# Kernel optimization log

Hardware: AMD Instinct MI355X
Metric: run time of the kernel (lower is better)

The kernel has to match this reference:

```python
import jax, jax.numpy as jnp
import numpy as np

N_NODES = 100000


def _gcn_conv(x, edge_index, W, b, n_nodes):
    # PyG GCNConv with add_self_loops=True, default gcn_norm:
    #   out = D^{-1/2} (A + I) D^{-1/2} (x @ W) + b
    xw = x @ W  # [N, out_dim]
    src = jnp.concatenate([edge_index[0], jnp.arange(n_nodes)])
    dst = jnp.concatenate([edge_index[1], jnp.arange(n_nodes)])
    ones = jnp.ones(src.shape[0], dtype=x.dtype)
    deg = jax.ops.segment_sum(ones, dst, num_segments=n_nodes)  # includes self loops
    dinv = jnp.where(deg > 0, jax.lax.rsqrt(deg), 0.0)
    norm = dinv[src] * dinv[dst]  # [E + N]
    msgs = xw[src] * norm[:, None]  # gather + scale per edge
    out = jax.ops.segment_sum(msgs, dst, num_segments=n_nodes)
    return out + b


def setup_inputs() -> dict:
    key = jax.random.key(0)
    k1, k2, k3, k4 = jax.random.split(key, 4)
    N, E = N_NODES, 1600000
    in_dim, hid_dim, out_dim = 128, 128, 64
    x = jax.random.normal(k1, (N, in_dim), dtype=jnp.float32)
    edge_index = jax.random.randint(k2, (2, E), 0, N, dtype=jnp.int64)
    W1 = jax.random.normal(k3, (in_dim, hid_dim), dtype=jnp.float32) * (1.0 / np.sqrt(in_dim))
    b1 = jnp.zeros((hid_dim,), dtype=jnp.float32)
    W2 = jax.random.normal(k4, (hid_dim, out_dim), dtype=jnp.float32) * (1.0 / np.sqrt(hid_dim))
    b2 = jnp.zeros((out_dim,), dtype=jnp.float32)
    return {"x": x, "edge_index": edge_index, "W1": W1, "b1": b1, "W2": W2, "b2": b2}


def reference(x, edge_index, W1, b1, W2, b2):
    h = _gcn_conv(x, edge_index, W1, b1, N_NODES)
    out = _gcn_conv(h, edge_index, W2, b2, N_NODES)
    return out
```

## Files before the change

### kernel.cpp

```cpp
#include <hip/hip_runtime.h>

#define NNODES 100000
#define NBUCK ((NNODES + 127) >> 7)
#define CAPB 3072
#define QCAP 1024
#define BINCAP 16
#define GFILL 256

typedef __attribute__((ext_vector_type(8))) short short8;
typedef __attribute__((ext_vector_type(4))) float f32x4;

__device__ __forceinline__ float bf2f(unsigned short u) {
    unsigned int v = ((unsigned int)u) << 16;
    return __builtin_bit_cast(float, v);
}
__device__ __forceinline__ unsigned short f2bf(float f) {
    unsigned int u = __builtin_bit_cast(unsigned int, f);
    u += 0x7FFF + ((u >> 16) & 1);
    return (unsigned short)(u >> 16);
}


__global__ __launch_bounds__(512) void fill_wc(const int* __restrict__ ei, int E,
                                               int* __restrict__ gcur,
                                               int* __restrict__ seg,
                                               int* __restrict__ deg) {
    __shared__ int lcnt[NBUCK];
    __shared__ int lbin[NBUCK * BINCAP];

    const int t = threadIdx.x;
    for (int i = t; i < NBUCK; i += 512) lcnt[i] = 0;
    __syncthreads();

    const int per = (E + GFILL - 1) / GFILL;
    const int e0 = blockIdx.x * per;
    const int e1 = min(e0 + per, E);

    for (int base = e0; base < e1; base += 512) {
        int e = base + t;
        if (e < e1) {
            int src = ei[e];
            int d = ei[E + e];
            atomicAdd(&deg[d], 1);
            int b = (unsigned)d >> 7;
            int p = (src << 7) | (d & 127);
            int pos = atomicAdd(&lcnt[b], 1);
            if (pos < BINCAP) {
                lbin[b * BINCAP + pos] = p;
            } else {
                int gp = atomicAdd(&gcur[b << 4], 1);
                if (gp < CAPB) seg[b * CAPB + gp] = p;
            }
        }
        __syncthreads();
        for (int bb = t; bb < NBUCK; bb += 512) {
            if (lcnt[bb] >= BINCAP) {
                int gp = atomicAdd(&gcur[bb << 4], BINCAP);
                if (gp + BINCAP <= CAPB) {
                    int* dp = seg + bb * CAPB + gp;
                    const int* sp = lbin + bb * BINCAP;
#pragma unroll
                    for (int j = 0; j < BINCAP; ++j) dp[j] = sp[j];
                }
                lcnt[bb] = 0;
            }
        }
        __syncthreads();
    }
    for (int bb = t; bb < NBUCK; bb += 512) {
        int c = min(lcnt[bb], BINCAP);
        if (c > 0) {
            int gp = atomicAdd(&gcur[bb << 4], c);
            int* dp = seg + bb * CAPB;
            const int* sp = lbin + bb * BINCAP;
            for (int j = 0; j < c && gp + j < CAPB; ++j) dp[gp + j] = sp[j];
        }
    }
}


__global__ __launch_bounds__(256) void w12_kernel(const float* __restrict__ W1,
                                                  const float* __restrict__ b1,
                                                  const float* __restrict__ W2,
                                                  float* __restrict__ W12,
                                                  float* __restrict__ bW2,
                                                  unsigned short* __restrict__ whi,
                                                  unsigned short* __restrict__ wlo) {
    int j = threadIdx.x % 64;
    int r = threadIdx.x / 64;
    if (blockIdx.x < 32) {
        int i = blockIdx.x * 4 + r;
        float acc = 0.f;
        for (int k = 0; k < 128; ++k) acc += W1[i * 128 + k] * W2[k * 64 + j];
        W12[i * 64 + j] = acc;
        int kc = i >> 5;
        int ik = i & 31;
        int lane = ((ik >> 3) << 4) | (j & 15);
        int jj = ik & 7;
        int nt = j >> 4;
        size_t idx = (size_t)(((nt << 2) | kc) * 64 + lane) * 8 + jj;
        unsigned short h = f2bf(acc);
        whi[idx] = h;
        wlo[idx] = f2bf(acc - bf2f(h));
    } else if (r == 0) {
        float acc = 0.f;
        for (int k = 0; k < 128; ++k) acc += b1[k] * W2[k * 64 + j];
        bW2[j] = acc;
    }
}


__global__ __launch_bounds__(256) void gemm_mfma(const float* __restrict__ X,
                                                 const unsigned short* __restrict__ whi,
                                                 const unsigned short* __restrict__ wlo,
                                                 const int* __restrict__ deg,
                                                 unsigned short* __restrict__ Ybf, int N) {
    const int tid = threadIdx.x;
    const int wv = tid >> 6;
    const int l = tid & 63;
    const int lm = l & 15;
    const int lk = l >> 4;
    const int rowbase = blockIdx.x * 64 + wv * 16;
    const int arow = min(rowbase + lm, N - 1);

    const float* xp = X + (size_t)arow * 128 + lk * 8;

    f32x4 acc[4];
#pragma unroll
    for (int nt = 0; nt < 4; ++nt) acc[nt] = (f32x4){0.f, 0.f, 0.f, 0.f};

#pragma unroll
    for (int kc = 0; kc < 4; ++kc) {
        float4 xa = *(const float4*)(xp + kc * 32);
        float4 xb = *(const float4*)(xp + kc * 32 + 4);
        float xs[8] = {xa.x, xa.y, xa.z, xa.w, xb.x, xb.y, xb.z, xb.w};
        short8 ah, al;
#pragma unroll
        for (int j = 0; j < 8; ++j) {
            unsigned short h = f2bf(xs[j]);
            ah[j] = (short)h;
            al[j] = (short)f2bf(xs[j] - bf2f(h));
        }
#pragma unroll
        for (int nt = 0; nt < 4; ++nt) {
            const size_t fb = (size_t)(((nt << 2) | kc) * 64 + l) * 8;
            short8 bh = *(const short8*)(whi + fb);
            short8 bl = *(const short8*)(wlo + fb);
            acc[nt] = __builtin_amdgcn_mfma_f32_16x16x32_bf16(ah, bh, acc[nt], 0, 0, 0);
            acc[nt] = __builtin_amdgcn_mfma_f32_16x16x32_bf16(ah, bl, acc[nt], 0, 0, 0);
            acc[nt] = __builtin_amdgcn_mfma_f32_16x16x32_bf16(al, bh, acc[nt], 0, 0, 0);
        }
    }

#pragma unroll
    for (int i = 0; i < 4; ++i) {
        int r = rowbase + lk * 4 + i;
        if (r < N) {
            float dv = rsqrtf((float)deg[r] + 1.0f);
#pragma unroll
            for (int nt = 0; nt < 4; ++nt)
                Ybf[(size_t)r * 64 + nt * 16 + lm] = f2bf(acc[nt][i] * dv);
        }
    }
}


__global__ __launch_bounds__(256, 8) void agg_q1(const int* __restrict__ gcur,
                                                 const int* __restrict__ seg,
                                                 const int* __restrict__ deg,
                                                 const unsigned short* __restrict__ Y,
                                                 int* __restrict__ qcsr,
                                                 unsigned short* __restrict__ out_bf, int N) {
    __shared__ int csrS[QCAP];
    __shared__ int rsS[32], cntS[32], curS[32];

    const int t = threadIdx.x;
    const int b = blockIdx.x >> 2;
    const int q = blockIdx.x & 3;
    const int nb = q << 5;

    if (t < 32) {
        int node = (b << 7) + nb + t;
        cntS[t] = (node < N) ? deg[node] : 0;
    }
    __syncthreads();
    if (t == 0) {
        int s = 0;
#pragma unroll
        for (int j = 0; j < 32; ++j) { rsS[j] = s; s += cntS[j]; }
    }
    __syncthreads();
    if (t < 32) curS[t] = rsS[t];
    __syncthreads();

    {
        const int total = min(gcur[b << 4], CAPB);
        const int* sp = seg + (size_t)b * CAPB;
        for (int i = t; i < total; i += 256) {
            int p = sp[i];
            int key = p & 127;
            if ((key >> 5) == q) {
                int pos = atomicAdd(&curS[key & 31], 1);
                if (pos < QCAP) csrS[pos] = (int)((unsigned)p >> 7);
            }
        }
    }
    __syncthreads();

    const int L = min(rsS[31] + cntS[31], QCAP);
    {
        int* dp = qcsr + ((size_t)((b << 2) | q) << 10);
        for (int i = t; i < L; i += 256) dp[i] = csrS[i];
    }

    const int g = t >> 3, lane = t & 7, c8 = lane * 8;
    const int node = (b << 7) + nb + g;
    if (node >= N) return;

    float a[8];
    {
        short8 sv = *(const short8*)(Y + (size_t)node * 64 + c8);
#pragma unroll
        for (int j = 0; j < 8; ++j) a[j] = bf2f((unsigned short)sv[j]);
    }

    const int ne = cntS[g];
    const int s0 = min(rsS[g], L);
    const int e0 = min(s0 + ne, L);
    int i = s0;

    for (; i + 8 <= e0; i += 8) {
        int a0 = csrS[i + 0];
        int a1 = csrS[i + 1];
        int a2 = csrS[i + 2];
        int a3 = csrS[i + 3];
        int a4 = csrS[i + 4];
        int a5 = csrS[i + 5];
        int a6 = csrS[i + 6];
        int a7 = csrS[i + 7];
        short8 v0 = *(const short8*)(Y + (size_t)a0 * 64 + c8);
        short8 v1 = *(const short8*)(Y + (size_t)a1 * 64 + c8);
        short8 v2 = *(const short8*)(Y + (size_t)a2 * 64 + c8);
        short8 v3 = *(const short8*)(Y + (size_t)a3 * 64 + c8);
        short8 v4 = *(const short8*)(Y + (size_t)a4 * 64 + c8);
        short8 v5 = *(const short8*)(Y + (size_t)a5 * 64 + c8);
        short8 v6 = *(const short8*)(Y + (size_t)a6 * 64 + c8);
        short8 v7 = *(const short8*)(Y + (size_t)a7 * 64 + c8);
#pragma unroll
        for (int j = 0; j < 8; ++j) {
            a[j] += bf2f((unsigned short)v0[j]) + bf2f((unsigned short)v1[j])
                  + bf2f((unsigned short)v2[j]) + bf2f((unsigned short)v3[j])
                  + bf2f((unsigned short)v4[j]) + bf2f((unsigned short)v5[j])
                  + bf2f((unsigned short)v6[j]) + bf2f((unsigned short)v7[j]);
        }
    }
    for (; i + 4 <= e0; i += 4) {
        int a0 = csrS[i + 0];
        int a1 = csrS[i + 1];
        int a2 = csrS[i + 2];
        int a3 = csrS[i + 3];
        short8 v0 = *(const short8*)(Y + (size_t)a0 * 64 + c8);
        short8 v1 = *(const short8*)(Y + (size_t)a1 * 64 + c8);
        short8 v2 = *(const short8*)(Y + (size_t)a2 * 64 + c8);
        short8 v3 = *(const short8*)(Y + (size_t)a3 * 64 + c8);
#pragma unroll
        for (int j = 0; j < 8; ++j) {
            a[j] += bf2f((unsigned short)v0[j]) + bf2f((unsigned short)v1[j])
                  + bf2f((unsigned short)v2[j]) + bf2f((unsigned short)v3[j]);
        }
    }
    for (; i < e0; ++i) {
        int aa = csrS[i];
        short8 vv = *(const short8*)(Y + (size_t)aa * 64 + c8);
#pragma unroll
        for (int j = 0; j < 8; ++j) a[j] += bf2f((unsigned short)vv[j]);
    }

    float di = rsqrtf((float)ne + 1.0f);
    float d2 = di * di;
    short8 o;
#pragma unroll
    for (int j = 0; j < 8; ++j) o[j] = (short)f2bf(d2 * a[j]);
    *(short8*)(out_bf + (size_t)node * 64 + c8) = o;
}


__global__ __launch_bounds__(256, 8) void agg_q2(const int* __restrict__ deg,
                                                 const int* __restrict__ qcsr,
                                                 const unsigned short* __restrict__ Y,
                                                 const float* __restrict__ bW2,
                                                 const float* __restrict__ b2,
                                                 float* __restrict__ out_f, int N) {
    __shared__ int csrS[QCAP];
    __shared__ int rsS[32], cntS[32];

    const int t = threadIdx.x;
    const int b = blockIdx.x >> 2;
    const int q = blockIdx.x & 3;
    const int nb = q << 5;

    if (t < 32) {
        int node = (b << 7) + nb + t;
        cntS[t] = (node < N) ? deg[node] : 0;
    }
    __syncthreads();
    if (t == 0) {
        int s = 0;
#pragma unroll
        for (int j = 0; j < 32; ++j) { rsS[j] = s; s += cntS[j]; }
    }
    __syncthreads();

    const int L = min(rsS[31] + cntS[31], QCAP);
    {
        const int* sp = qcsr + ((size_t)((b << 2) | q) << 10);
        for (int i = t; i < L; i += 256) csrS[i] = sp[i];
    }
    __syncthreads();

    const int g = t >> 3, lane = t & 7, c8 = lane * 8;
    const int node = (b << 7) + nb + g;
    if (node >= N) return;

    float a[8];
    {
        short8 sv = *(const short8*)(Y + (size_t)node * 64 + c8);
#pragma unroll
        for (int j = 0; j < 8; ++j) a[j] = bf2f((unsigned short)sv[j]);
    }
    float ds = 0.f;

    const int ne = cntS[g];
    const int s0 = min(rsS[g], L);
    const int e0 = min(s0 + ne, L);
    int i = s0;

    for (; i + 8 <= e0; i += 8) {
        int a0 = csrS[i + 0];
        int a1 = csrS[i + 1];
        int a2 = csrS[i + 2];
        int a3 = csrS[i + 3];
        int a4 = csrS[i + 4];
        int a5 = csrS[i + 5];
        int a6 = csrS[i + 6];
        int a7 = csrS[i + 7];
        short8 v0 = *(const short8*)(Y + (size_t)a0 * 64 + c8);
        short8 v1 = *(const short8*)(Y + (size_t)a1 * 64 + c8);
        short8 v2 = *(const short8*)(Y + (size_t)a2 * 64 + c8);
        short8 v3 = *(const short8*)(Y + (size_t)a3 * 64 + c8);
        short8 v4 = *(const short8*)(Y + (size_t)a4 * 64 + c8);
        short8 v5 = *(const short8*)(Y + (size_t)a5 * 64 + c8);
        short8 v6 = *(const short8*)(Y + (size_t)a6 * 64 + c8);
        short8 v7 = *(const short8*)(Y + (size_t)a7 * 64 + c8);
        ds += rsqrtf((float)deg[csrS[i + lane]] + 1.0f);
#pragma unroll
        for (int j = 0; j < 8; ++j) {
            a[j] += bf2f((unsigned short)v0[j]) + bf2f((unsigned short)v1[j])
                  + bf2f((unsigned short)v2[j]) + bf2f((unsigned short)v3[j])
                  + bf2f((unsigned short)v4[j]) + bf2f((unsigned short)v5[j])
                  + bf2f((unsigned short)v6[j]) + bf2f((unsigned short)v7[j]);
        }
    }
    for (; i + 4 <= e0; i += 4) {
        int a0 = csrS[i + 0];
        int a1 = csrS[i + 1];
        int a2 = csrS[i + 2];
        int a3 = csrS[i + 3];
        short8 v0 = *(const short8*)(Y + (size_t)a0 * 64 + c8);
        short8 v1 = *(const short8*)(Y + (size_t)a1 * 64 + c8);
        short8 v2 = *(const short8*)(Y + (size_t)a2 * 64 + c8);
        short8 v3 = *(const short8*)(Y + (size_t)a3 * 64 + c8);
        if (lane < 4) ds += rsqrtf((float)deg[csrS[i + lane]] + 1.0f);
#pragma unroll
        for (int j = 0; j < 8; ++j) {
            a[j] += bf2f((unsigned short)v0[j]) + bf2f((unsigned short)v1[j])
                  + bf2f((unsigned short)v2[j]) + bf2f((unsigned short)v3[j]);
        }
    }
    for (; i < e0; ++i) {
        int aa = csrS[i];
        short8 vv = *(const short8*)(Y + (size_t)aa * 64 + c8);
        if (lane == 0) ds += rsqrtf((float)deg[aa] + 1.0f);
#pragma unroll
        for (int j = 0; j < 8; ++j) a[j] += bf2f((unsigned short)vv[j]);
    }

    float di = rsqrtf((float)ne + 1.0f);
    float dt = ds;
    dt += __shfl_xor(dt, 1, 64);
    dt += __shfl_xor(dt, 2, 64);
    dt += __shfl_xor(dt, 4, 64);
    float si = di * (di + dt);
    float4 bb0 = *(const float4*)(bW2 + c8);
    float4 bb1 = *(const float4*)(bW2 + c8 + 4);
    float4 bv0 = *(const float4*)(b2 + c8);
    float4 bv1 = *(const float4*)(b2 + c8 + 4);
    float4 o0, o1;
    o0.x = di * a[0] + si * bb0.x + bv0.x;
    o0.y = di * a[1] + si * bb0.y + bv0.y;
    o0.z = di * a[2] + si * bb0.z + bv0.z;
    o0.w = di * a[3] + si * bb0.w + bv0.w;
    o1.x = di * a[4] + si * bb1.x + bv1.x;
    o1.y = di * a[5] + si * bb1.y + bv1.y;
    o1.z = di * a[6] + si * bb1.z + bv1.z;
    o1.w = di * a[7] + si * bb1.w + bv1.w;
    *(float4*)(out_f + (size_t)node * 64 + c8) = o0;
    *(float4*)(out_f + (size_t)node * 64 + c8 + 4) = o1;
}


extern "C" void kernel_launch(void* const* d_in, const int* in_sizes, int n_in,
                              void* d_out, int out_size, void* d_ws, size_t ws_size,
                              hipStream_t stream) {
    const float* x  = (const float*)d_in[0];
    const int*   ei = (const int*)d_in[1];
    const float* W1 = (const float*)d_in[2];
    const float* b1 = (const float*)d_in[3];
    const float* W2 = (const float*)d_in[4];
    const float* b2 = (const float*)d_in[5];
    float* out = (float*)d_out;

    const int N = NNODES;
    const int E = in_sizes[1] / 2;

    float* ws   = (float*)d_ws;
    float* W12  = ws;
    float* bW2  = W12 + 8192;
    unsigned short* whi = (unsigned short*)(bW2 + 64);
    unsigned short* wlo = whi + 8192;
    unsigned short* ybf = wlo + 8192;
    unsigned short* zbf = ybf + (size_t)N * 64;
    int*  seg  = (int*)(zbf + (size_t)N * 64);
    int*  gcur = seg + (size_t)NBUCK * CAPB;
    int*  deg  = gcur + (size_t)NBUCK * 16;
    int*  qcsr = deg + (size_t)NBUCK * 128;

    hipMemsetAsync(gcur, 0, (size_t)NBUCK * (16 + 128) * sizeof(int), stream);

    fill_wc<<<GFILL, 512, 0, stream>>>(ei, E, gcur, seg, deg);
    w12_kernel<<<33, 256, 0, stream>>>(W1, b1, W2, W12, bW2, whi, wlo);

    gemm_mfma<<<(N + 63) / 64, 256, 0, stream>>>(x, whi, wlo, deg, ybf, N);
    agg_q1<<<NBUCK * 4, 256, 0, stream>>>(gcur, seg, deg, ybf, qcsr, zbf, N);
    agg_q2<<<NBUCK * 4, 256, 0, stream>>>(deg, qcsr, zbf, bW2, b2, out, N);
}
```

Baseline: 263.7 us.

## Compute degrees per bucket from binned edges and precompute inverse-sqrt degrees

Removes the 1.6M global atomicAdds on the degree array from the edge-binning kernel. A new per-bucket stats kernel now counts degrees with shared-memory atomics over the binned segments and writes both deg and a precomputed dinv array. The GEMM and second aggregation read dinv directly instead of recomputing rsqrt from deg per neighbour. This costs an extra kernel launch and another pass over the segment buffer, and the memset shrinks because deg no longer needs zeroing.

```diff
diff --git a/kernel.cpp b/kernel.cpp
--- a/kernel.cpp
+++ b/kernel.cpp
@@ -23,8 +23,7 @@
 
 __global__ __launch_bounds__(512) void fill_wc(const int* __restrict__ ei, int E,
                                                int* __restrict__ gcur,
-                                               int* __restrict__ seg,
-                                               int* __restrict__ deg) {
+                                               int* __restrict__ seg) {
     __shared__ int lcnt[NBUCK];
     __shared__ int lbin[NBUCK * BINCAP];
 
@@ -41,7 +40,6 @@
         if (e < e1) {
             int src = ei[e];
             int d = ei[E + e];
-            atomicAdd(&deg[d], 1);
             int b = (unsigned)d >> 7;
             int p = (src << 7) | (d & 127);
             int pos = atomicAdd(&lcnt[b], 1);
@@ -75,6 +73,26 @@
             const int* sp = lbin + bb * BINCAP;
             for (int j = 0; j < c && gp + j < CAPB; ++j) dp[gp + j] = sp[j];
         }
+    }
+}
+
+
+__global__ __launch_bounds__(256) void stats_kernel(const int* __restrict__ gcur,
+                                                    const int* __restrict__ seg,
+                                                    int* __restrict__ deg,
+                                                    float* __restrict__ dinv, int N) {
+    __shared__ int cnt[128];
+    const int t = threadIdx.x, b = blockIdx.x;
+    if (t < 128) cnt[t] = 0;
+    __syncthreads();
+    int c = min(gcur[b << 4], CAPB);
+    const int* sp = seg + (size_t)b * CAPB;
+    for (int i = t; i < c; i += 256) atomicAdd(&cnt[sp[i] & 127], 1);
+    __syncthreads();
+    if (t < 128) {
+        deg[b * 128 + t] = cnt[t];
+        int node = (b << 7) + t;
+        if (node < N) dinv[node] = rsqrtf((float)cnt[t] + 1.0f);
     }
 }
 
@@ -113,7 +131,7 @@
 __global__ __launch_bounds__(256) void gemm_mfma(const float* __restrict__ X,
                                                  const unsigned short* __restrict__ whi,
                                                  const unsigned short* __restrict__ wlo,
-                                                 const int* __restrict__ deg,
+                                                 const float* __restrict__ dinv,
                                                  unsigned short* __restrict__ Ybf, int N) {
     const int tid = threadIdx.x;
     const int wv = tid >> 6;
@@ -156,7 +174,7 @@
     for (int i = 0; i < 4; ++i) {
         int r = rowbase + lk * 4 + i;
         if (r < N) {
-            float dv = rsqrtf((float)deg[r] + 1.0f);
+            float dv = dinv[r];
 #pragma unroll
             for (int nt = 0; nt < 4; ++nt)
                 Ybf[(size_t)r * 64 + nt * 16 + lm] = f2bf(acc[nt][i] * dv);
@@ -179,10 +197,7 @@
     const int q = blockIdx.x & 3;
     const int nb = q << 5;
 
-    if (t < 32) {
-        int node = (b << 7) + nb + t;
-        cntS[t] = (node < N) ? deg[node] : 0;
-    }
+    if (t < 32) cntS[t] = deg[b * 128 + nb + t];
     __syncthreads();
     if (t == 0) {
         int s = 0;
@@ -286,6 +301,7 @@
 
 
 __global__ __launch_bounds__(256, 8) void agg_q2(const int* __restrict__ deg,
+                                                 const float* __restrict__ dinv,
                                                  const int* __restrict__ qcsr,
                                                  const unsigned short* __restrict__ Y,
                                                  const float* __restrict__ bW2,
@@ -299,10 +315,7 @@
     const int q = blockIdx.x & 3;
     const int nb = q << 5;
 
-    if (t < 32) {
-        int node = (b << 7) + nb + t;
-        cntS[t] = (node < N) ? deg[node] : 0;
-    }
+    if (t < 32) cntS[t] = deg[b * 128 + nb + t];
     __syncthreads();
     if (t == 0) {
         int s = 0;
@@ -352,7 +365,7 @@
         short8 v5 = *(const short8*)(Y + (size_t)a5 * 64 + c8);
         short8 v6 = *(const short8*)(Y + (size_t)a6 * 64 + c8);
         short8 v7 = *(const short8*)(Y + (size_t)a7 * 64 + c8);
-        ds += rsqrtf((float)deg[csrS[i + lane]] + 1.0f);
+        ds += dinv[csrS[i + lane]];
 #pragma unroll
         for (int j = 0; j < 8; ++j) {
             a[j] += bf2f((unsigned short)v0[j]) + bf2f((unsigned short)v1[j])
@@ -370,7 +383,7 @@
         short8 v1 = *(const short8*)(Y + (size_t)a1 * 64 + c8);
         short8 v2 = *(const short8*)(Y + (size_t)a2 * 64 + c8);
         short8 v3 = *(const short8*)(Y + (size_t)a3 * 64 + c8);
-        if (lane < 4) ds += rsqrtf((float)deg[csrS[i + lane]] + 1.0f);
+        if (lane < 4) ds += dinv[csrS[i + lane]];
 #pragma unroll
         for (int j = 0; j < 8; ++j) {
             a[j] += bf2f((unsigned short)v0[j]) + bf2f((unsigned short)v1[j])
@@ -380,7 +393,7 @@
     for (; i < e0; ++i) {
         int aa = csrS[i];
         short8 vv = *(const short8*)(Y + (size_t)aa * 64 + c8);
-        if (lane == 0) ds += rsqrtf((float)deg[aa] + 1.0f);
+        if (lane == 0) ds += dinv[aa];
 #pragma unroll
         for (int j = 0; j < 8; ++j) a[j] += bf2f((unsigned short)vv[j]);
     }
@@ -424,7 +437,8 @@
     const int E = in_sizes[1] / 2;
 
     float* ws   = (float*)d_ws;
-    float* W12  = ws;
+    float* dinv = ws;
+    float* W12  = dinv + N;
     float* bW2  = W12 + 8192;
     unsigned short* whi = (unsigned short*)(bW2 + 64);
     unsigned short* wlo = whi + 8192;
@@ -435,12 +449,13 @@
     int*  deg  = gcur + (size_t)NBUCK * 16;
     int*  qcsr = deg + (size_t)NBUCK * 128;
 
-    hipMemsetAsync(gcur, 0, (size_t)NBUCK * (16 + 128) * sizeof(int), stream);
-
-    fill_wc<<<GFILL, 512, 0, stream>>>(ei, E, gcur, seg, deg);
+    hipMemsetAsync(gcur, 0, (size_t)NBUCK * 16 * sizeof(int), stream);
+
+    fill_wc<<<GFILL, 512, 0, stream>>>(ei, E, gcur, seg);
     w12_kernel<<<33, 256, 0, stream>>>(W1, b1, W2, W12, bW2, whi, wlo);
-
-    gemm_mfma<<<(N + 63) / 64, 256, 0, stream>>>(x, whi, wlo, deg, ybf, N);
+    stats_kernel<<<NBUCK, 256, 0, stream>>>(gcur, seg, deg, dinv, N);
+
+    gemm_mfma<<<(N + 63) / 64, 256, 0, stream>>>(x, whi, wlo, dinv, ybf, N);
     agg_q1<<<NBUCK * 4, 256, 0, stream>>>(gcur, seg, deg, ybf, qcsr, zbf, N);
-    agg_q2<<<NBUCK * 4, 256, 0, stream>>>(deg, qcsr, zbf, bW2, b2, out, N);
-}
+    agg_q2<<<NBUCK * 4, 256, 0, stream>>>(deg, dinv, qcsr, zbf, bW2, b2, out, N);
+}
```

New measurement: 215.3 us. 1.22x faster.
